# Optimization experiments

Hardware: AMD Instinct MI355X
Metric: run time of the kernel (lower is better)

Reference implementation:

```python
import jax, jax.numpy as jnp
import numpy as np

V, B, NT, EN, EMB, ODIM = 5000, 512, 50, 200, 200, 40
PERP = 30.0
BETA_TEMP = 0.2
SINKHORN_ALPHA = 20.0
WEIGHT_ECR = 250.0
ECR_ITERS = 100
SNE_ITERS = 20
EPS_DIV = 1e-16


def _pairwise_sq(x, y):
    # ||x_i||^2 + ||y_j||^2 - 2 x_i . y_j  (matches module's pairwise_euclidean_distance)
    return (jnp.sum(x * x, axis=1)[:, None] + jnp.sum(y * y, axis=1)[None, :]
            - 2.0 * (x @ y.T))


def _bn_train(x, g, b):
    # BatchNorm1d, training mode: batch statistics, biased variance
    m = x.mean(axis=0)
    v = x.var(axis=0)
    return (x - m) / jnp.sqrt(v + 1e-5) * g + b


def _snekhorn_reduce(X, proj):
    # SNEkhorn-style symmetric entropic affinity on rows of X (log-domain
    # symmetric Sinkhorn with uniform marginals), followed by a linear readout
    # to ODIM dims. X: (n, d) -> (n, ODIM).
    C = _pairwise_sq(X, X)                       # (n, n)
    n = X.shape[0]
    eps = jnp.mean(C) / jnp.log(PERP) + 1e-6     # bandwidth tied to perplexity
    log_a = -jnp.log(float(n))                   # uniform target marginal

    @jax.checkpoint
    def step(f, _):
        lse = jax.nn.logsumexp((f[None, :] - C) / eps, axis=1)
        f = 0.5 * (f + eps * (log_a - lse))      # symmetric Sinkhorn update
        return f, None

    f, _ = jax.lax.scan(step, jnp.zeros(n, C.dtype), None, length=SNE_ITERS)
    P = jnp.exp((f[:, None] + f[None, :] - C) / eps)  # (n, n) affinity
    return P @ proj                                   # (n, ODIM)


def _ecr_loss(cost):
    # ECR: entropic OT between topic and word embeddings (fixed-iteration Sinkhorn)
    Km = jnp.exp(-cost * SINKHORN_ALPHA)          # (NT, V)
    a = jnp.full((NT, 1), 1.0 / NT, cost.dtype)
    bm = jnp.full((V, 1), 1.0 / V, cost.dtype)

    def step(u, _):
        v = bm / (Km.T @ u + EPS_DIV)
        u = a / (Km @ v + EPS_DIV)
        return u, None

    u, _ = jax.lax.scan(step, jnp.full((NT, 1), 1.0 / NT, cost.dtype), None,
                        length=ECR_ITERS)
    v = bm / (Km.T @ u + EPS_DIV)
    transp = u * (Km * v.T)
    return WEIGHT_ECR * jnp.sum(transp * cost)


def setup_inputs() -> dict:
    key = jax.random.key(0)
    ks = jax.random.split(key, 12)

    def nrm(k, shape, s=0.02):
        return jax.random.normal(k, shape, jnp.float32) * s

    word_emb = jax.random.normal(ks[0], (V, EMB), jnp.float32)
    word_emb = word_emb / jnp.linalg.norm(word_emb, axis=1, keepdims=True)
    topic_emb = jax.random.normal(ks[1], (NT, EMB), jnp.float32) * 0.1
    topic_emb = topic_emb / jnp.linalg.norm(topic_emb, axis=1, keepdims=True)

    return dict(
        bow=jax.random.uniform(ks[2], (B, V), jnp.float32),
        eps_noise=jax.random.normal(ks[3], (ODIM, NT), jnp.float32),
        W1=nrm(ks[4], (EN, V)), b1=jnp.zeros(EN, jnp.float32),
        W2=nrm(ks[5], (EN, EN)), b2=jnp.zeros(EN, jnp.float32),
        Wmu=nrm(ks[6], (NT, EN)), bmu=jnp.zeros(NT, jnp.float32),
        Wlv=nrm(ks[7], (NT, EN)), blv=jnp.zeros(NT, jnp.float32),
        g_mu=jnp.ones(NT, jnp.float32), be_mu=jnp.zeros(NT, jnp.float32),
        g_lv=jnp.ones(NT, jnp.float32), be_lv=jnp.zeros(NT, jnp.float32),
        g_dec=jnp.ones(V, jnp.float32), be_dec=jnp.zeros(V, jnp.float32),
        word_emb=word_emb, topic_emb=topic_emb,
        proj_V=nrm(ks[8], (V, ODIM), 1.0),
        proj_K=nrm(ks[9], (NT, ODIM), 1.0),
    )


def reference(bow, eps_noise, W1, b1, W2, b2, Wmu, bmu, Wlv, blv,
              g_mu, be_mu, g_lv, be_lv, g_dec, be_dec,
              word_emb, topic_emb, proj_V, proj_K):
    # bow_reduced = SNEkhorn(bow.T).T : (ODIM, V)
    bow_reduced = _snekhorn_reduce(bow.T, proj_V).T

    # encoder1: Linear -> softplus -> Linear -> softplus
    e1 = jax.nn.softplus(bow_reduced @ W1.T + b1)
    e1 = jax.nn.softplus(e1 @ W2.T + b2)
    mu = _bn_train(e1 @ Wmu.T + bmu, g_mu, be_mu)        # (ODIM, NT)
    logvar = _bn_train(e1 @ Wlv.T + blv, g_lv, be_lv)

    z = mu + eps_noise * jnp.exp(0.5 * logvar)           # reparameterize (training)
    theta = jax.nn.softmax(z, axis=1)                    # (ODIM, NT)
    theta_reduced = _snekhorn_reduce(theta.T, proj_K).T  # (ODIM, NT)

    # KL vs logistic-normal prior; with a = ones: mu2 = 0, var2 = 1 - 1/NT
    var2 = 1.0 - 1.0 / NT
    var = jnp.exp(logvar)
    kld = 0.5 * ((var / var2 + mu * mu / var2 + jnp.log(var2) - logvar).sum(axis=1) - NT)
    loss_KL = kld.mean()

    # beta + decode (cost computed once; torch code computes it twice identically)
    cost = _pairwise_sq(topic_emb, word_emb)             # (NT, V)
    beta = jax.nn.softmax(-cost / BETA_TEMP, axis=0)
    recon = jax.nn.softmax(_bn_train(theta_reduced @ beta, g_dec, be_dec), axis=-1)
    recon_loss = -(bow_reduced * jnp.log(recon)).sum(axis=1).mean()

    loss_TM = recon_loss + loss_KL
    loss_ECR = _ecr_loss(cost)
    loss = loss_TM + loss_ECR
    return loss, loss_TM, loss_ECR, theta_reduced
```

## Files before the change

kernel.cpp:

```cpp
#include <hip/hip_runtime.h>
#include <hip/hip_bf16.h>
#include <hip/hip_fp16.h>

#define VV 5000
#define NTOP 50
#define ENH 200
#define NEMB 200
#define OD 40
#define MP 5120
#define KNS 5008

typedef __attribute__((ext_vector_type(8))) short short8;
typedef __attribute__((ext_vector_type(4))) float f32x4;

constexpr size_t OFF_R      = 0;
constexpr size_t OFF_S      = 20224;
constexpr size_t OFF_SCAL   = 22528;
constexpr size_t OFF_PHIA   = 22784;
constexpr size_t OFF_PHIB   = 43008;
constexpr size_t OFF_ROWS   = 63232;
constexpr size_t OFF_PARTS  = 63744;
constexpr size_t OFF_FLAGS  = 71936;
constexpr size_t OFF_MUPRE  = 72960;
constexpr size_t OFF_LVPRE  = 81152;
constexpr size_t OFF_E1T    = 89344;
constexpr size_t OFF_E2T    = 121600;
constexpr size_t OFF_THRED  = 153856;
constexpr size_t OFF_BOWRED = 162048;
constexpr size_t ZERO_BYTES = 962304;
constexpr size_t OFF_PVT    = 962304;
constexpr size_t OFF_XB     = 1453824;
constexpr size_t OFF_CE     = 6696704;
constexpr size_t OFF_COST   = 56696832;
constexpr size_t OFF_KM     = 57697024;
constexpr size_t OFF_BETA   = 58697216;
constexpr size_t OFF_RN     = 59697408;

__global__ __launch_bounds__(256) void k1_stats(const float* __restrict__ bow,
    __hip_bfloat16* __restrict__ Xb, float* __restrict__ r, float* __restrict__ s){
  __shared__ float lds[64][129];
  const int t = threadIdx.x;
  const int i0 = blockIdx.x * 128, d0 = blockIdx.y * 64;
  #pragma unroll
  for (int m = 0; m < 32; ++m){
    int idx = m*256 + t;
    int di = idx >> 7;
    int ii = idx & 127;
    int gi = i0 + ii;
    lds[di][ii] = (gi < VV) ? bow[(size_t)(d0+di)*VV + gi] : 0.f;
  }
  __syncthreads();
  if (t < 128 && (i0 + t) < VV){
    float acc = 0.f;
    for (int di = 0; di < 64; ++di){ float v = lds[di][t]; acc += v*v; }
    atomicAdd(&r[i0+t], acc);
  }
  if (t < 64){
    float acc = 0.f;
    for (int ii = 0; ii < 128; ++ii) acc += lds[t][ii];
    atomicAdd(&s[d0+t], acc);
  }
  __syncthreads();
  #pragma unroll
  for (int m = 0; m < 32; ++m){
    int idx = m*256 + t;
    int ii = idx >> 6;
    int dd = idx & 63;
    Xb[(size_t)(i0+ii)*512 + d0 + dd] = __float2bfloat16(lds[dd][ii]);
  }
}

__global__ __launch_bounds__(256) void k2_eps(const float* __restrict__ r,
    const float* __restrict__ s, float* __restrict__ scal){
  const int t = threadIdx.x;
  float a = 0.f, b = 0.f;
  for (int i = t; i < VV; i += 256) a += r[i];
  for (int d = t; d < 512; d += 256){ float v = s[d]; b += v*v; }
  #pragma unroll
  for (int off = 32; off; off >>= 1){
    a += __shfl_down(a, off, 64);
    b += __shfl_down(b, off, 64);
  }
  __shared__ float ra[4], rb[4];
  int lane = t & 63, w = t >> 6;
  if (lane == 0){ ra[w] = a; rb[w] = b; }
  __syncthreads();
  if (t == 0){
    float sa = ra[0]+ra[1]+ra[2]+ra[3];
    float sb = rb[0]+rb[1]+rb[2]+rb[3];
    float meanC = 2.f*sa/(float)VV - 2.f*sb/((float)VV*(float)VV);
    float eps = meanC / logf(30.f) + 1e-6f;
    scal[0] = eps;
    scal[1] = 1.f/eps;
  }
}

__device__ __forceinline__ void ecr_block(int b, int it_base, int n_iters, bool do_final,
    const __half* __restrict__ Kn, const float* __restrict__ cost,
    float* __restrict__ acc, int* __restrict__ cnt, float* __restrict__ scal,
    char* smem){
  __half* KmL = (__half*)smem;
  float* varr = (float*)(smem + 32208);
  float* us   = (float*)(smem + 33488);
  float* p5   = (float*)(smem + 33696);
  float* redr = (float*)(smem + 34736);
  const int t = threadIdx.x;
  const int base = (b < 8) ? b*313 : 2504 + (b-8)*312;
  const int sz   = (b < 8) ? 313 : 312;
  for (int c = t; c < 322; c += 256){
    if (c < sz){
      #pragma unroll
      for (int q = 0; q < NTOP; ++q)
        KmL[q*322 + c] = Kn[(size_t)q*KNS + base + c];
    } else {
      #pragma unroll
      for (int q = 0; q < NTOP; ++q) KmL[q*322 + c] = __float2half(0.f);
    }
  }
  if (t < 52){
    float u0 = 0.f;
    if (t < NTOP){
      if (it_base == 0) u0 = 1.f/(float)NTOP;
      else {
        float sm = __hip_atomic_load(&acc[((it_base-1)%3)*64 + t],
                                     __ATOMIC_RELAXED, __HIP_MEMORY_SCOPE_AGENT);
        u0 = (1.f/(float)NTOP)/(sm + 1e-16f);
      }
    }
    us[t] = u0;
  }
  for (int c = sz + t; c < 320; c += 256) varr[c] = 0.f;
  __syncthreads();
  const bool act = (2*t < sz);
  for (int k = 0; k < n_iters; ++k){
    const int g = it_base + k;
    if (act){
      float w0 = 0.f, w1 = 0.f, w2 = 0.f, w3 = 0.f;
      #pragma unroll
      for (int q = 0; q < NTOP; q += 2){
        float u0 = us[q], u1 = us[q+1];
        float2 f0 = __half22float2(*(const __half2*)(KmL + q*322 + 2*t));
        float2 f1 = __half22float2(*(const __half2*)(KmL + (q+1)*322 + 2*t));
        w0 += f0.x*u0; w1 += f0.y*u0;
        w2 += f1.x*u1; w3 += f1.y*u1;
      }
      float2 vv;
      vv.x = (1.f/(float)VV)/((w0+w2) + 1e-16f);
      vv.y = (2*t+1 < sz) ? (1.f/(float)VV)/((w1+w3) + 1e-16f) : 0.f;
      *(float2*)(varr + 2*t) = vv;
    }
    __syncthreads();
    if (t < 250){
      const int qq = t % NTOP, stripe = t / NTOP;
      const __half* kp = KmL + qq*322 + stripe*64;
      const float* vp = varr + stripe*64;
      float s0 = 0.f, s1 = 0.f, s2 = 0.f, s3 = 0.f;
      #pragma unroll
      for (int n = 0; n < 64; n += 4){
        float2 fa = __half22float2(*(const __half2*)(kp + n));
        float2 fb = __half22float2(*(const __half2*)(kp + n + 2));
        float4 v4 = *(const float4*)(vp + n);
        s0 += fa.x*v4.x; s1 += fa.y*v4.y; s2 += fb.x*v4.z; s3 += fb.y*v4.w;
      }
      p5[stripe*52 + qq] = (s0+s1)+(s2+s3);
    }
    __syncthreads();
    if (t < NTOP){
      float sm = p5[t] + p5[52+t] + p5[104+t] + p5[156+t] + p5[208+t];
      __hip_atomic_fetch_add(&acc[(g%3)*64 + t], sm,
                             __ATOMIC_RELAXED, __HIP_MEMORY_SCOPE_AGENT);
    }
    __asm__ volatile("s_waitcnt vmcnt(0)" ::: "memory");
    if (t == 0){
      __hip_atomic_fetch_add(cnt, 1, __ATOMIC_RELEASE, __HIP_MEMORY_SCOPE_AGENT);
      const int tgt = 16*(g+1);
      while (__hip_atomic_load(cnt, __ATOMIC_ACQUIRE, __HIP_MEMORY_SCOPE_AGENT) < tgt)
        __builtin_amdgcn_s_sleep(1);
    }
    if (t < NTOP){
      float sm = __hip_atomic_load(&acc[(g%3)*64 + t],
                                   __ATOMIC_RELAXED, __HIP_MEMORY_SCOPE_AGENT);
      us[t] = (1.f/(float)NTOP)/(sm + 1e-16f);
    }
    if (t < 64)
      __hip_atomic_store(&acc[((g+2)%3)*64 + t], 0.f,
                         __ATOMIC_RELAXED, __HIP_MEMORY_SCOPE_AGENT);
    __syncthreads();
  }
  if (!do_final) return;
  float lsum = 0.f;
  if (act){
    float w0 = 0.f, w1 = 0.f, w2 = 0.f, w3 = 0.f;
    #pragma unroll
    for (int q = 0; q < NTOP; q += 2){
      float u0 = us[q], u1 = us[q+1];
      float2 f0 = __half22float2(*(const __half2*)(KmL + q*322 + 2*t));
      float2 f1 = __half22float2(*(const __half2*)(KmL + (q+1)*322 + 2*t));
      w0 += f0.x*u0; w1 += f0.y*u0;
      w2 += f1.x*u1; w3 += f1.y*u1;
    }
    float v0 = (1.f/(float)VV)/((w0+w2) + 1e-16f);
    const bool ok1 = (2*t+1 < sz);
    float v1 = ok1 ? (1.f/(float)VV)/((w1+w3) + 1e-16f) : 0.f;
    float accv = 0.f;
    #pragma unroll
    for (int q = 0; q < NTOP; ++q){
      float2 f = __half22float2(*(const __half2*)(KmL + q*322 + 2*t));
      float uq = us[q];
      float c0 = cost[(size_t)q*VV + base + 2*t];
      accv += uq*f.x*v0*c0;
      if (ok1){
        float c1 = cost[(size_t)q*VV + base + 2*t + 1];
        accv += uq*f.y*v1*c1;
      }
    }
    lsum = accv;
  }
  #pragma unroll
  for (int off = 32; off; off >>= 1) lsum += __shfl_down(lsum, off, 64);
  if ((t & 63) == 0) redr[t >> 6] = lsum;
  __syncthreads();
  if (t == 0) atomicAdd(&scal[3], redr[0]+redr[1]+redr[2]+redr[3]);
}

__global__ __launch_bounds__(256) void k3_gemm_ecr(const __hip_bfloat16* __restrict__ Xb,
    const float* __restrict__ r, float* __restrict__ scal, __half* __restrict__ Ce,
    const __half* __restrict__ Kn, const float* __restrict__ cost,
    float* __restrict__ accg, int* __restrict__ cnt){
  __shared__ __align__(16) char smem[36864];
  if (blockIdx.x < 16){
    ecr_block(blockIdx.x, 0, 12, false, Kn, cost, accg, cnt, scal, smem);
    return;
  }
  __hip_bfloat16* As = (__hip_bfloat16*)smem;
  __hip_bfloat16* Bs = (__hip_bfloat16*)(smem + 128*72*2);
  const int b2 = blockIdx.x - 16;
  const int t = threadIdx.x;
  const int i0 = (b2 % 40) * 128, j0 = (b2 / 40) * 128;
  const int lane = t & 63, w = t >> 6;
  const int wr = w >> 1, wc = w & 1;
  const int m16 = lane & 15, q4 = lane >> 4;
  f32x4 acc[4][4];
  #pragma unroll
  for (int a = 0; a < 4; ++a)
    #pragma unroll
    for (int b = 0; b < 4; ++b) acc[a][b] = (f32x4){0.f,0.f,0.f,0.f};
  const int srow = t >> 3, sseg = t & 7;
  for (int kc = 0; kc < 512; kc += 64){
    __syncthreads();
    #pragma unroll
    for (int m = 0; m < 4; ++m){
      int row = m*32 + srow;
      uint4 va = *(const uint4*)(Xb + (size_t)(i0+row)*512 + kc + sseg*8);
      *(uint4*)(As + row*72 + sseg*8) = va;
      uint4 vb = *(const uint4*)(Xb + (size_t)(j0+row)*512 + kc + sseg*8);
      *(uint4*)(Bs + row*72 + sseg*8) = vb;
    }
    __syncthreads();
    #pragma unroll
    for (int ks = 0; ks < 64; ks += 32){
      short8 af[4], bf[4];
      #pragma unroll
      for (int f = 0; f < 4; ++f){
        af[f] = *(const short8*)(As + (wr*64 + f*16 + m16)*72 + ks + q4*8);
        bf[f] = *(const short8*)(Bs + (wc*64 + f*16 + m16)*72 + ks + q4*8);
      }
      #pragma unroll
      for (int fr = 0; fr < 4; ++fr)
        #pragma unroll
        for (int fc = 0; fc < 4; ++fc)
          acc[fr][fc] = __builtin_amdgcn_mfma_f32_16x16x32_bf16(af[fr], bf[fc], acc[fr][fc], 0, 0, 0);
    }
  }
  const float inv_eps = scal[1];
  #pragma unroll
  for (int fr = 0; fr < 4; ++fr){
    int rbase = i0 + wr*64 + fr*16 + q4*4;
    #pragma unroll
    for (int fc = 0; fc < 4; ++fc){
      int col = j0 + wc*64 + fc*16 + m16;
      if (col < VV){
        float rc = r[col];
        #pragma unroll
        for (int q = 0; q < 4; ++q){
          int row = rbase + q;
          if (row < VV){
            float val = (r[row] + rc - 2.f*acc[fr][fc][q]) * inv_eps;
            Ce[(size_t)row*VV + col] = __float2half(val);
          }
        }
      }
    }
  }
}

__global__ __launch_bounds__(256) void k4_sweep_ecr(const __half* __restrict__ Ce,
    const float* __restrict__ phi_in, float* __restrict__ phi_out,
    const __half* __restrict__ Kn, const float* __restrict__ cost,
    float* __restrict__ accg, int* __restrict__ cnt, float* __restrict__ scal,
    int it_base, int n_ecr){
  __shared__ __align__(16) char smem[34752];
  const int t = threadIdx.x;
  if (blockIdx.x < 16){
    ecr_block(blockIdx.x, it_base, n_ecr, it_base + n_ecr == 100,
              Kn, cost, accg, cnt, scal, smem);
    return;
  }
  const int i0 = (blockIdx.x - 16) * 4;
  float acc[4] = {0.f, 0.f, 0.f, 0.f};
  const uint4* ce0 = (const uint4*)(Ce + (size_t)i0*VV);
  for (int u = t; u < 625; u += 256){
    float4 p0 = *(const float4*)(phi_in + u*8);
    float4 p1 = *(const float4*)(phi_in + u*8 + 4);
    #pragma unroll
    for (int rr = 0; rr < 4; ++rr){
      uint4 v = ce0[(size_t)rr*625 + u];
      const __half2* hp = (const __half2*)&v;
      float2 c0 = __half22float2(hp[0]);
      float2 c1 = __half22float2(hp[1]);
      float2 c2 = __half22float2(hp[2]);
      float2 c3 = __half22float2(hp[3]);
      acc[rr] += __expf(p0.x - c0.x) + __expf(p0.y - c0.y)
               + __expf(p0.z - c1.x) + __expf(p0.w - c1.y)
               + __expf(p1.x - c2.x) + __expf(p1.y - c2.y)
               + __expf(p1.z - c3.x) + __expf(p1.w - c3.y);
    }
  }
  #pragma unroll
  for (int rr = 0; rr < 4; ++rr)
    #pragma unroll
    for (int off = 32; off; off >>= 1)
      acc[rr] += __shfl_down(acc[rr], off, 64);
  float* red = (float*)smem;
  int lane = t & 63, w = t >> 6;
  if (lane == 0){
    #pragma unroll
    for (int rr = 0; rr < 4; ++rr) red[w*4 + rr] = acc[rr];
  }
  __syncthreads();
  if (t < 4){
    float ssum = red[t] + red[4+t] + red[8+t] + red[12+t];
    const float loga = -8.517193191416238f;
    phi_out[i0 + t] = 0.5f*(phi_in[i0 + t] + loga - __logf(ssum));
  }
}

__global__ __launch_bounds__(256) void k5p_pvt(const float* __restrict__ projV,
    __hip_bfloat16* __restrict__ pvt){
  int idx = blockIdx.x*256 + threadIdx.x;
  if (idx >= 48*MP) return;
  int n = idx / MP, j = idx - n*MP;
  float v = (n < OD && j < VV) ? projV[(size_t)j*OD + n] : 0.f;
  pvt[idx] = __float2bfloat16(v);
}

__global__ __launch_bounds__(256) void k5_bowred(const __half* __restrict__ Ce,
    const float* __restrict__ phi, const __hip_bfloat16* __restrict__ pvt,
    float* __restrict__ brpA, float* __restrict__ brpB){
  __shared__ __align__(16) char smem[25600];
  __hip_bfloat16* As = (__hip_bfloat16*)smem;
  __hip_bfloat16* Bs = (__hip_bfloat16*)(smem + 18432);
  const int t = threadIdx.x;
  const int i0 = blockIdx.x * 128;
  const int k0 = blockIdx.y * 640;
  const int lane = t & 63, w = t >> 6;
  const int m16 = lane & 15, q4 = lane >> 4;
  f32x4 acc[2][3];
  #pragma unroll
  for (int a = 0; a < 2; ++a)
    #pragma unroll
    for (int b = 0; b < 3; ++b) acc[a][b] = (f32x4){0.f,0.f,0.f,0.f};
  for (int kc = k0; kc < k0 + 640; kc += 64){
    __syncthreads();
    #pragma unroll
    for (int m = 0; m < 4; ++m){
      int g = m*256 + t;
      int row = g >> 3, cg = g & 7;
      int gi = i0 + row, j2 = kc + cg*8;
      union { __hip_bfloat16 h[8]; short8 v; } u;
      if (gi < VV && j2 < VV){
        uint4 vce = *(const uint4*)(Ce + (size_t)gi*VV + j2);
        const __half2* hp = (const __half2*)&vce;
        float pb = phi[gi];
        float4 pj0 = *(const float4*)(phi + j2);
        float4 pj1 = *(const float4*)(phi + j2 + 4);
        float pj[8] = {pj0.x,pj0.y,pj0.z,pj0.w,pj1.x,pj1.y,pj1.z,pj1.w};
        #pragma unroll
        for (int e = 0; e < 4; ++e){
          float2 ce = __half22float2(hp[e]);
          u.h[2*e]   = __float2bfloat16(__expf(pb + pj[2*e]   - ce.x));
          u.h[2*e+1] = __float2bfloat16(__expf(pb + pj[2*e+1] - ce.y));
        }
      } else {
        #pragma unroll
        for (int e = 0; e < 8; ++e) u.h[e] = __float2bfloat16(0.f);
      }
      *(short8*)(As + row*72 + cg*8) = u.v;
    }
    #pragma unroll
    for (int m = 0; m < 12; ++m){
      int idx = m*256 + t;
      int row = idx >> 6, c = idx & 63;
      Bs[row*72 + c] = pvt[(size_t)row*MP + kc + c];
    }
    __syncthreads();
    #pragma unroll
    for (int ks = 0; ks < 64; ks += 32){
      short8 af[2], bf[3];
      #pragma unroll
      for (int f = 0; f < 2; ++f)
        af[f] = *(const short8*)(As + (w*32 + f*16 + m16)*72 + ks + q4*8);
      #pragma unroll
      for (int f = 0; f < 3; ++f)
        bf[f] = *(const short8*)(Bs + (f*16 + m16)*72 + ks + q4*8);
      #pragma unroll
      for (int fr = 0; fr < 2; ++fr)
        #pragma unroll
        for (int fc = 0; fc < 3; ++fc)
          acc[fr][fc] = __builtin_amdgcn_mfma_f32_16x16x32_bf16(af[fr], bf[fc], acc[fr][fc], 0, 0, 0);
    }
  }
  __syncthreads();
  float* LF = (float*)smem;
  #pragma unroll
  for (int fr = 0; fr < 2; ++fr){
    int lr = w*32 + fr*16 + q4*4;
    #pragma unroll
    for (int fc = 0; fc < 3; ++fc){
      int col = fc*16 + m16;
      #pragma unroll
      for (int q = 0; q < 4; ++q)
        LF[col*133 + lr + q] = acc[fr][fc][q];
    }
  }
  __syncthreads();
  float* brp = (blockIdx.y < 6) ? brpA + (size_t)blockIdx.y*200000
                                : brpB + (size_t)(blockIdx.y - 6)*200000;
  for (int o = t; o < OD*128; o += 256){
    int col = o >> 7, row = o & 127;
    int gr = i0 + row;
    if (gr < VV) brp[(size_t)col*VV + gr] = LF[col*133 + row];
  }
}

__global__ __launch_bounds__(256) void k5r_red(const float* __restrict__ brpA,
    const float* __restrict__ brpB, float* __restrict__ br){
  int idx = blockIdx.x*256 + threadIdx.x;
  if (idx >= 50000) return;
  const float4* a = (const float4*)brpA;
  const float4* b = (const float4*)brpB;
  float4 s = a[idx];
  #pragma unroll
  for (int sl = 1; sl < 6; ++sl){
    float4 v = a[(size_t)sl*50000 + idx];
    s.x += v.x; s.y += v.y; s.z += v.z; s.w += v.w;
  }
  #pragma unroll
  for (int sl = 0; sl < 2; ++sl){
    float4 v = b[(size_t)sl*50000 + idx];
    s.x += v.x; s.y += v.y; s.z += v.z; s.w += v.w;
  }
  ((float4*)br)[idx] = s;
}

__global__ __launch_bounds__(256) void k6_e1(const float* __restrict__ br,
    const float* __restrict__ W1, float* __restrict__ e1pre){
  const int t = threadIdx.x;
  const int lane = t & 63, w = t >> 6;
  const int k = blockIdx.x*4 + w;
  const int f0 = blockIdx.y * 125;
  float acc[OD];
  #pragma unroll
  for (int i = 0; i < OD; ++i) acc[i] = 0.f;
  const float4* w4p = (const float4*)(W1 + (size_t)k*VV);
  for (int f4 = f0 + lane; f4 < f0 + 125; f4 += 64){
    float4 wv = w4p[f4];
    #pragma unroll
    for (int i = 0; i < OD; ++i){
      float4 bv = ((const float4*)(br + (size_t)i*VV))[f4];
      acc[i] += bv.x*wv.x + bv.y*wv.y + bv.z*wv.z + bv.w*wv.w;
    }
  }
  #pragma unroll
  for (int i = 0; i < OD; ++i)
    #pragma unroll
    for (int off = 32; off; off >>= 1)
      acc[i] += __shfl_down(acc[i], off, 64);
  __shared__ float red[4][OD];
  if (lane == 0){
    #pragma unroll
    for (int i = 0; i < OD; ++i) red[w][i] = acc[i];
  }
  __syncthreads();
  if (t < 160){
    int ww = t / OD, i = t - ww*OD;
    int kk = blockIdx.x*4 + ww;
    atomicAdd(&e1pre[kk*OD + i], red[ww][i]);
  }
}

__global__ __launch_bounds__(256) void k6b_sp(const float* __restrict__ b1,
    float* __restrict__ e1t){
  int idx = blockIdx.x*256 + threadIdx.x;
  if (idx >= ENH*OD) return;
  int kk = idx / OD;
  float x = e1t[idx] + b1[kk];
  e1t[idx] = (x > 20.f) ? x : log1pf(__expf(x));
}

__global__ __launch_bounds__(256) void k7_e2(const float* __restrict__ e1t,
    const float* __restrict__ W2, const float* __restrict__ b2, float* __restrict__ e2t){
  const int t = threadIdx.x;
  const int lane = t & 63, w = t >> 6;
  const int k = blockIdx.x*4 + w;
  float acc[OD];
  #pragma unroll
  for (int i = 0; i < OD; ++i) acc[i] = 0.f;
  for (int j = lane; j < ENH; j += 64){
    float wv = W2[(size_t)k*ENH + j];
    #pragma unroll
    for (int i = 0; i < OD; ++i) acc[i] += e1t[j*OD + i] * wv;
  }
  #pragma unroll
  for (int i = 0; i < OD; ++i)
    #pragma unroll
    for (int off = 32; off; off >>= 1)
      acc[i] += __shfl_down(acc[i], off, 64);
  __shared__ float red[4][OD];
  if (lane == 0){
    #pragma unroll
    for (int i = 0; i < OD; ++i) red[w][i] = acc[i];
  }
  __syncthreads();
  if (t < 160){
    int ww = t / OD, i = t - ww*OD;
    int kk = blockIdx.x*4 + ww;
    float x = red[ww][i] + b2[kk];
    float sp = (x > 20.f) ? x : log1pf(__expf(x));
    e2t[kk*OD + i] = sp;
  }
}

__global__ __launch_bounds__(256) void k8a_mulv(const float* __restrict__ e2t,
    const float* __restrict__ Wmu, const float* __restrict__ bmu,
    const float* __restrict__ Wlv, const float* __restrict__ blv,
    float* __restrict__ mupre, float* __restrict__ lvpre){
  int id = blockIdx.x*256 + threadIdx.x;
  if (id >= NTOP*OD) return;
  int t50 = id / OD, i = id - t50*OD;
  float am = 0.f, al = 0.f;
  for (int kk = 0; kk < ENH; ++kk){
    float e = e2t[kk*OD + i];
    am += e * Wmu[t50*ENH + kk];
    al += e * Wlv[t50*ENH + kk];
  }
  mupre[t50*OD + i] = am + bmu[t50];
  lvpre[t50*OD + i] = al + blv[t50];
}

__global__ __launch_bounds__(256) void k8b_theta(const float* __restrict__ mupre,
    const float* __restrict__ lvpre,
    const float* __restrict__ g_mu, const float* __restrict__ be_mu,
    const float* __restrict__ g_lv, const float* __restrict__ be_lv,
    const float* __restrict__ eps_noise, const float* __restrict__ projK,
    float* __restrict__ thred, float* __restrict__ d_out3, float* __restrict__ scal){
  __shared__ float mu[NTOP][OD];
  __shared__ float lv[NTOP][OD];
  __shared__ float th[OD][NTOP];
  __shared__ float C2[NTOP][NTOP];
  __shared__ float P2[NTOP][NTOP];
  __shared__ float f2[NTOP], nf[NTOP];
  __shared__ float sred[4];
  __shared__ float eps2s[2];
  const int t = threadIdx.x;
  if (t < NTOP){
    float m = 0.f;
    for (int i = 0; i < OD; ++i) m += mupre[t*OD + i];
    m *= (1.f/OD);
    float v = 0.f;
    for (int i = 0; i < OD; ++i){ float d = mupre[t*OD+i] - m; v += d*d; }
    v *= (1.f/OD);
    float sc = g_mu[t] * rsqrtf(v + 1e-5f);
    float sh = be_mu[t];
    for (int i = 0; i < OD; ++i) mu[t][i] = (mupre[t*OD+i] - m)*sc + sh;
    m = 0.f;
    for (int i = 0; i < OD; ++i) m += lvpre[t*OD + i];
    m *= (1.f/OD);
    v = 0.f;
    for (int i = 0; i < OD; ++i){ float d = lvpre[t*OD+i] - m; v += d*d; }
    v *= (1.f/OD);
    sc = g_lv[t] * rsqrtf(v + 1e-5f);
    sh = be_lv[t];
    for (int i = 0; i < OD; ++i) lv[t][i] = (lvpre[t*OD+i] - m)*sc + sh;
  }
  __syncthreads();
  {
    float kl = 0.f;
    if (t < OD){
      const float var2 = 1.f - 1.f/(float)NTOP;
      const float lv2 = logf(var2);
      float ssum = 0.f;
      for (int q = 0; q < NTOP; ++q){
        float l = lv[q][t];
        float m = mu[q][t];
        ssum += (__expf(l) + m*m)/var2 + lv2 - l;
      }
      kl = 0.5f*(ssum - (float)NTOP);
    }
    #pragma unroll
    for (int off = 32; off; off >>= 1) kl += __shfl_down(kl, off, 64);
    if ((t & 63) == 0) sred[t >> 6] = kl;
    __syncthreads();
    if (t == 0) scal[2] = (sred[0]+sred[1]+sred[2]+sred[3]) * (1.f/OD);
    __syncthreads();
  }
  if (t < OD){
    float z[NTOP];
    float mx = -1e30f;
    for (int q = 0; q < NTOP; ++q){
      float val = mu[q][t] + eps_noise[t*NTOP + q]*__expf(0.5f*lv[q][t]);
      z[q] = val;
      mx = fmaxf(mx, val);
    }
    float ssum = 0.f;
    for (int q = 0; q < NTOP; ++q){ float e = __expf(z[q]-mx); z[q] = e; ssum += e; }
    float inv = 1.f/ssum;
    for (int q = 0; q < NTOP; ++q) th[t][q] = z[q]*inv;
  }
  __syncthreads();
  {
    float csum = 0.f;
    for (int pr = t; pr < NTOP*NTOP; pr += 256){
      int a = pr / NTOP, b = pr - (pr/NTOP)*NTOP;
      float ss = 0.f;
      for (int i = 0; i < OD; ++i){ float d = th[i][a] - th[i][b]; ss += d*d; }
      C2[a][b] = ss;
      csum += ss;
    }
    #pragma unroll
    for (int off = 32; off; off >>= 1) csum += __shfl_down(csum, off, 64);
    if ((t & 63) == 0) sred[t >> 6] = csum;
    __syncthreads();
    if (t == 0){
      float meanC = (sred[0]+sred[1]+sred[2]+sred[3]) / ((float)NTOP*NTOP);
      float e2 = meanC / logf(30.f) + 1e-6f;
      eps2s[0] = e2; eps2s[1] = 1.f/e2;
    }
  }
  if (t < NTOP) f2[t] = 0.f;
  __syncthreads();
  const float loga2 = -logf((float)NTOP);
  for (int it = 0; it < 20; ++it){
    if (t < NTOP){
      float ie = eps2s[1];
      float ssum = 0.f;
      for (int sI = 0; sI < NTOP; ++sI)
        ssum += __expf((f2[sI] - C2[t][sI]) * ie);
      float lse = __logf(ssum);
      nf[t] = 0.5f*(f2[t] + eps2s[0]*(loga2 - lse));
    }
    __syncthreads();
    if (t < NTOP) f2[t] = nf[t];
    __syncthreads();
  }
  for (int pr = t; pr < NTOP*NTOP; pr += 256){
    int a = pr / NTOP, b = pr - (pr/NTOP)*NTOP;
    P2[a][b] = __expf((f2[a] + f2[b] - C2[a][b]) * eps2s[1]);
  }
  __syncthreads();
  for (int o = t; o < NTOP*OD; o += 256){
    int t50 = o / OD, kk = o - (o/OD)*OD;
    float ssum = 0.f;
    for (int sI = 0; sI < NTOP; ++sI)
      ssum += P2[t50][sI] * projK[sI*OD + kk];
    thred[kk*NTOP + t50] = ssum;
    d_out3[kk*NTOP + t50] = ssum;
  }
}

__global__ __launch_bounds__(256) void k10_cost(const float* __restrict__ temb,
    const float* __restrict__ wemb, float* __restrict__ cost, __half* __restrict__ Kn,
    float* __restrict__ beta){
  __shared__ float Tt[100][52];
  __shared__ float wed[100][68];
  __shared__ float sc[52][64];
  __shared__ float tn[52];
  __shared__ float wn[64];
  const int t = threadIdx.x;
  const int j0 = blockIdx.x * 64;
  const int tg = t >> 4, jg = t & 15;
  float am[4][4];
  #pragma unroll
  for (int a = 0; a < 4; ++a)
    #pragma unroll
    for (int b = 0; b < 4; ++b) am[a][b] = 0.f;
  float tnp = 0.f, wnp = 0.f;
  for (int c = 0; c < 2; ++c){
    __syncthreads();
    const int dbase = c*100;
    for (int idx = t; idx < NTOP*100; idx += 256){
      int t50 = idx / 100, d = idx - t50*100;
      Tt[d][t50] = temb[t50*NEMB + dbase + d];
    }
    for (int idx = t; idx < 64*100; idx += 256){
      int j = idx / 100, d = idx - j*100;
      int gj = j0 + j;
      wed[d][j] = (gj < VV) ? wemb[(size_t)gj*NEMB + dbase + d] : 0.f;
    }
    __syncthreads();
    if (t < NTOP){
      float a = 0.f;
      for (int d = 0; d < 100; ++d){ float v = Tt[d][t]; a += v*v; }
      tnp += a;
    }
    if (t >= 64 && t < 128){
      int j = t - 64;
      float a = 0.f;
      for (int d = 0; d < 100; ++d){ float v = wed[d][j]; a += v*v; }
      wnp += a;
    }
    if (t < 208){
      for (int d = 0; d < 100; ++d){
        const float4 tv = *(const float4*)(&Tt[d][tg*4]);
        const float4 wv = *(const float4*)(&wed[d][jg*4]);
        am[0][0] += tv.x*wv.x; am[0][1] += tv.x*wv.y; am[0][2] += tv.x*wv.z; am[0][3] += tv.x*wv.w;
        am[1][0] += tv.y*wv.x; am[1][1] += tv.y*wv.y; am[1][2] += tv.y*wv.z; am[1][3] += tv.y*wv.w;
        am[2][0] += tv.z*wv.x; am[2][1] += tv.z*wv.y; am[2][2] += tv.z*wv.z; am[2][3] += tv.z*wv.w;
        am[3][0] += tv.w*wv.x; am[3][1] += tv.w*wv.y; am[3][2] += tv.w*wv.z; am[3][3] += tv.w*wv.w;
      }
    }
  }
  if (t < NTOP) tn[t] = tnp;
  if (t >= 64 && t < 128) wn[t-64] = wnp;
  __syncthreads();
  if (t < 208){
    #pragma unroll
    for (int a = 0; a < 4; ++a){
      int t50 = tg*4 + a;
      if (t50 < NTOP){
        float tv = tn[t50];
        float cc[4];
        #pragma unroll
        for (int b = 0; b < 4; ++b) cc[b] = tv + wn[jg*4+b] - 2.f*am[a][b];
        int gj = j0 + jg*4;
        if (gj + 3 < VV)
          *(float4*)(cost + (size_t)t50*VV + gj) = make_float4(cc[0],cc[1],cc[2],cc[3]);
        #pragma unroll
        for (int b = 0; b < 4; ++b) sc[t50][jg*4+b] = -5.f*cc[b];
      }
    }
  }
  __syncthreads();
  if (t < 64){
    int gj = j0 + t;
    if (gj < VV){
      float mx = -1e30f;
      for (int q = 0; q < NTOP; ++q) mx = fmaxf(mx, sc[q][t]);
      float ssum = 0.f;
      for (int q = 0; q < NTOP; ++q){ float e = __expf(sc[q][t]-mx); sc[q][t] = e; ssum += e; }
      float inv = 1.f/ssum;
      for (int q = 0; q < NTOP; ++q){
        float e = sc[q][t];
        float e2 = e*e;
        Kn[(size_t)q*KNS + gj] = __float2half(e2*e2);
        beta[(size_t)q*VV + gj] = e*inv;
      }
    }
  }
}

__global__ __launch_bounds__(256) void k12_reconA(const float* __restrict__ thred,
    const float* __restrict__ beta, const float* __restrict__ g_dec,
    const float* __restrict__ be_dec, float* __restrict__ Rn){
  __shared__ float trs[OD][NTOP];
  const int t = threadIdx.x;
  for (int o = t; o < OD*NTOP; o += 256) trs[o/NTOP][o - (o/NTOP)*NTOP] = thred[o];
  __syncthreads();
  int j = blockIdx.x*256 + t;
  if (j >= VV) return;
  float a[OD];
  #pragma unroll
  for (int i = 0; i < OD; ++i) a[i] = 0.f;
  for (int q = 0; q < NTOP; ++q){
    float bv = beta[(size_t)q*VV + j];
    #pragma unroll
    for (int i = 0; i < OD; ++i) a[i] += trs[i][q]*bv;
  }
  float m = 0.f;
  #pragma unroll
  for (int i = 0; i < OD; ++i) m += a[i];
  m *= (1.f/OD);
  float v = 0.f;
  #pragma unroll
  for (int i = 0; i < OD; ++i){ float d = a[i]-m; v += d*d; }
  v *= (1.f/OD);
  float scale = g_dec[j]*rsqrtf(v + 1e-5f);
  float sh = be_dec[j];
  #pragma unroll
  for (int i = 0; i < OD; ++i) Rn[(size_t)i*VV + j] = (a[i]-m)*scale + sh;
}

__global__ __launch_bounds__(256) void k13_reconB(const float* __restrict__ Rn,
    const float* __restrict__ br, float* __restrict__ rows){
  const int i = blockIdx.x;
  const int t = threadIdx.x;
  float s1 = 0.f, s2 = 0.f, s3 = 0.f;
  for (int j = t; j < VV; j += 256){
    float rn = Rn[(size_t)i*VV + j];
    float bv = br[(size_t)i*VV + j];
    s1 += __expf(rn);
    s2 += bv*rn;
    s3 += bv;
  }
  #pragma unroll
  for (int off = 32; off; off >>= 1){
    s1 += __shfl_down(s1, off, 64);
    s2 += __shfl_down(s2, off, 64);
    s3 += __shfl_down(s3, off, 64);
  }
  __shared__ float red[3][4];
  int lane = t & 63, w = t >> 6;
  if (lane == 0){ red[0][w] = s1; red[1][w] = s2; red[2][w] = s3; }
  __syncthreads();
  if (t == 0){
    rows[i]      = red[0][0]+red[0][1]+red[0][2]+red[0][3];
    rows[40 + i] = red[1][0]+red[1][1]+red[1][2]+red[1][3];
    rows[80 + i] = red[2][0]+red[2][1]+red[2][2]+red[2][3];
  }
}

__global__ void k14_final(const float* __restrict__ rows, const float* __restrict__ scal,
    float* __restrict__ out){
  const int t = threadIdx.x;
  float v = 0.f;
  if (t < OD) v = rows[40 + t] - logf(rows[t]) * rows[80 + t];
  #pragma unroll
  for (int off = 32; off; off >>= 1) v += __shfl_down(v, off, 64);
  if (t == 0){
    float recon = -v * (1.f/OD);
    float tm = recon + scal[2];
    float ecr = 250.f * scal[3];
    out[0] = tm + ecr;
    out[1] = tm;
    out[2] = ecr;
  }
}

extern "C" void kernel_launch(void* const* d_in, const int* in_sizes, int n_in,
                              void* d_out, int out_size, void* d_ws, size_t ws_size,
                              hipStream_t stream){
  const float* bow   = (const float*)d_in[0];
  const float* epsn  = (const float*)d_in[1];
  const float* W1    = (const float*)d_in[2];
  const float* b1    = (const float*)d_in[3];
  const float* W2    = (const float*)d_in[4];
  const float* b2    = (const float*)d_in[5];
  const float* Wmu   = (const float*)d_in[6];
  const float* bmu   = (const float*)d_in[7];
  const float* Wlv   = (const float*)d_in[8];
  const float* blv   = (const float*)d_in[9];
  const float* g_mu  = (const float*)d_in[10];
  const float* be_mu = (const float*)d_in[11];
  const float* g_lv  = (const float*)d_in[12];
  const float* be_lv = (const float*)d_in[13];
  const float* g_dec = (const float*)d_in[14];
  const float* be_dec= (const float*)d_in[15];
  const float* wemb  = (const float*)d_in[16];
  const float* temb  = (const float*)d_in[17];
  const float* projV = (const float*)d_in[18];
  const float* projK = (const float*)d_in[19];
  char* ws = (char*)d_ws;
  float* r     = (float*)(ws + OFF_R);
  float* s     = (float*)(ws + OFF_S);
  float* scal  = (float*)(ws + OFF_SCAL);
  float* phiA  = (float*)(ws + OFF_PHIA);
  float* phiB  = (float*)(ws + OFF_PHIB);
  float* rows  = (float*)(ws + OFF_ROWS);
  float* accg  = (float*)(ws + OFF_PARTS);
  int*   cnt   = (int*)(ws + OFF_FLAGS);
  float* mupre = (float*)(ws + OFF_MUPRE);
  float* lvpre = (float*)(ws + OFF_LVPRE);
  float* e1t   = (float*)(ws + OFF_E1T);
  float* e2t   = (float*)(ws + OFF_E2T);
  float* thred = (float*)(ws + OFF_THRED);
  float* br    = (float*)(ws + OFF_BOWRED);
  __hip_bfloat16* pvt = (__hip_bfloat16*)(ws + OFF_PVT);
  __hip_bfloat16* Xb  = (__hip_bfloat16*)(ws + OFF_XB);
  __half* Ce   = (__half*)(ws + OFF_CE);
  float* cost  = (float*)(ws + OFF_COST);
  __half* Kn   = (__half*)(ws + OFF_KM);
  float* beta  = (float*)(ws + OFF_BETA);
  float* Rn    = (float*)(ws + OFF_RN);
  float* brpA  = (float*)(ws + OFF_XB);
  float* brpB  = (float*)(ws + OFF_COST);
  float* out   = (float*)d_out;

  hipMemsetAsync(d_ws, 0, ZERO_BYTES, stream);
  k10_cost<<<79, 256, 0, stream>>>(temb, wemb, cost, Kn, beta);
  k1_stats<<<dim3(40, 8), 256, 0, stream>>>(bow, Xb, r, s);
  k2_eps<<<1, 256, 0, stream>>>(r, s, scal);
  k3_gemm_ecr<<<1616, 256, 0, stream>>>(Xb, r, scal, Ce, Kn, cost, accg, cnt);
  {
    float* pin = phiA; float* pout = phiB;
    int itb = 12;
    for (int itr = 0; itr < 20; ++itr){
      int n = (itr < 12) ? 4 : 5;
      k4_sweep_ecr<<<1266, 256, 0, stream>>>(Ce, pin, pout, Kn, cost, accg, cnt,
                                             scal, itb, n);
      itb += n;
      float* tmp = pin; pin = pout; pout = tmp;
    }
  }
  k5p_pvt<<<960, 256, 0, stream>>>(projV, pvt);
  k5_bowred<<<dim3(40, 8), 256, 0, stream>>>(Ce, phiA, pvt, brpA, brpB);
  k5r_red<<<196, 256, 0, stream>>>(brpA, brpB, br);
  k6_e1<<<dim3(50, 10), 256, 0, stream>>>(br, W1, e1t);
  k6b_sp<<<32, 256, 0, stream>>>(b1, e1t);
  k7_e2<<<50, 256, 0, stream>>>(e1t, W2, b2, e2t);
  k8a_mulv<<<8, 256, 0, stream>>>(e2t, Wmu, bmu, Wlv, blv, mupre, lvpre);
  k8b_theta<<<1, 256, 0, stream>>>(mupre, lvpre, g_mu, be_mu, g_lv, be_lv,
                                   epsn, projK, thred, out + 3, scal);
  k12_reconA<<<20, 256, 0, stream>>>(thred, beta, g_dec, be_dec, Rn);
  k13_reconB<<<40, 256, 0, stream>>>(Rn, br, rows);
  k14_final<<<1, 64, 0, stream>>>(rows, scal, out);
}
```

Baseline: 845.8 us.

## Redistribute ECR Sinkhorn iterations across more kernels and widen sweep rows per block

```diff
diff --git a/kernel.cpp b/kernel.cpp
--- a/kernel.cpp
+++ b/kernel.cpp
@@ -36,65 +36,6 @@
 constexpr size_t OFF_BETA   = 58697216;
 constexpr size_t OFF_RN     = 59697408;
 
-__global__ __launch_bounds__(256) void k1_stats(const float* __restrict__ bow,
-    __hip_bfloat16* __restrict__ Xb, float* __restrict__ r, float* __restrict__ s){
-  __shared__ float lds[64][129];
-  const int t = threadIdx.x;
-  const int i0 = blockIdx.x * 128, d0 = blockIdx.y * 64;
-  #pragma unroll
-  for (int m = 0; m < 32; ++m){
-    int idx = m*256 + t;
-    int di = idx >> 7;
-    int ii = idx & 127;
-    int gi = i0 + ii;
-    lds[di][ii] = (gi < VV) ? bow[(size_t)(d0+di)*VV + gi] : 0.f;
-  }
-  __syncthreads();
-  if (t < 128 && (i0 + t) < VV){
-    float acc = 0.f;
-    for (int di = 0; di < 64; ++di){ float v = lds[di][t]; acc += v*v; }
-    atomicAdd(&r[i0+t], acc);
-  }
-  if (t < 64){
-    float acc = 0.f;
-    for (int ii = 0; ii < 128; ++ii) acc += lds[t][ii];
-    atomicAdd(&s[d0+t], acc);
-  }
-  __syncthreads();
-  #pragma unroll
-  for (int m = 0; m < 32; ++m){
-    int idx = m*256 + t;
-    int ii = idx >> 6;
-    int dd = idx & 63;
-    Xb[(size_t)(i0+ii)*512 + d0 + dd] = __float2bfloat16(lds[dd][ii]);
-  }
-}
-
-__global__ __launch_bounds__(256) void k2_eps(const float* __restrict__ r,
-    const float* __restrict__ s, float* __restrict__ scal){
-  const int t = threadIdx.x;
-  float a = 0.f, b = 0.f;
-  for (int i = t; i < VV; i += 256) a += r[i];
-  for (int d = t; d < 512; d += 256){ float v = s[d]; b += v*v; }
-  #pragma unroll
-  for (int off = 32; off; off >>= 1){
-    a += __shfl_down(a, off, 64);
-    b += __shfl_down(b, off, 64);
-  }
-  __shared__ float ra[4], rb[4];
-  int lane = t & 63, w = t >> 6;
-  if (lane == 0){ ra[w] = a; rb[w] = b; }
-  __syncthreads();
-  if (t == 0){
-    float sa = ra[0]+ra[1]+ra[2]+ra[3];
-    float sb = rb[0]+rb[1]+rb[2]+rb[3];
-    float meanC = 2.f*sa/(float)VV - 2.f*sb/((float)VV*(float)VV);
-    float eps = meanC / logf(30.f) + 1e-6f;
-    scal[0] = eps;
-    scal[1] = 1.f/eps;
-  }
-}
-
 __device__ __forceinline__ void ecr_block(int b, int it_base, int n_iters, bool do_final,
     const __half* __restrict__ Kn, const float* __restrict__ cost,
     float* __restrict__ acc, int* __restrict__ cnt, float* __restrict__ scal,
@@ -223,13 +164,80 @@
   if (t == 0) atomicAdd(&scal[3], redr[0]+redr[1]+redr[2]+redr[3]);
 }
 
+__global__ __launch_bounds__(256) void k1_stats(const float* __restrict__ bow,
+    __hip_bfloat16* __restrict__ Xb, float* __restrict__ r, float* __restrict__ s,
+    const __half* __restrict__ Kn, const float* __restrict__ cost,
+    float* __restrict__ accg, int* __restrict__ cnt, float* __restrict__ scal){
+  __shared__ __align__(16) char smem[34816];
+  const int t = threadIdx.x;
+  if (blockIdx.x >= 40){
+    int b = (blockIdx.x - 40)*8 + blockIdx.y;
+    ecr_block(b, 0, 15, false, Kn, cost, accg, cnt, scal, smem);
+    return;
+  }
+  float (*lds)[129] = (float(*)[129])smem;
+  const int i0 = blockIdx.x * 128, d0 = blockIdx.y * 64;
+  #pragma unroll
+  for (int m = 0; m < 32; ++m){
+    int idx = m*256 + t;
+    int di = idx >> 7;
+    int ii = idx & 127;
+    int gi = i0 + ii;
+    lds[di][ii] = (gi < VV) ? bow[(size_t)(d0+di)*VV + gi] : 0.f;
+  }
+  __syncthreads();
+  if (t < 128 && (i0 + t) < VV){
+    float acc = 0.f;
+    for (int di = 0; di < 64; ++di){ float v = lds[di][t]; acc += v*v; }
+    atomicAdd(&r[i0+t], acc);
+  }
+  if (t < 64){
+    float acc = 0.f;
+    for (int ii = 0; ii < 128; ++ii) acc += lds[t][ii];
+    atomicAdd(&s[d0+t], acc);
+  }
+  __syncthreads();
+  #pragma unroll
+  for (int m = 0; m < 32; ++m){
+    int idx = m*256 + t;
+    int ii = idx >> 6;
+    int dd = idx & 63;
+    Xb[(size_t)(i0+ii)*512 + d0 + dd] = __float2bfloat16(lds[dd][ii]);
+  }
+}
+
+__global__ __launch_bounds__(256) void k2_eps(const float* __restrict__ r,
+    const float* __restrict__ s, float* __restrict__ scal){
+  const int t = threadIdx.x;
+  float a = 0.f, b = 0.f;
+  for (int i = t; i < VV; i += 256) a += r[i];
+  for (int d = t; d < 512; d += 256){ float v = s[d]; b += v*v; }
+  #pragma unroll
+  for (int off = 32; off; off >>= 1){
+    a += __shfl_down(a, off, 64);
+    b += __shfl_down(b, off, 64);
+  }
+  __shared__ float ra[4], rb[4];
+  int lane = t & 63, w = t >> 6;
+  if (lane == 0){ ra[w] = a; rb[w] = b; }
+  __syncthreads();
+  if (t == 0){
+    float sa = ra[0]+ra[1]+ra[2]+ra[3];
+    float sb = rb[0]+rb[1]+rb[2]+rb[3];
+    float meanC = 2.f*sa/(float)VV - 2.f*sb/((float)VV*(float)VV);
+    float eps = meanC / logf(30.f) + 1e-6f;
+    scal[0] = eps;
+    scal[1] = 1.f/eps;
+  }
+}
+
 __global__ __launch_bounds__(256) void k3_gemm_ecr(const __hip_bfloat16* __restrict__ Xb,
     const float* __restrict__ r, float* __restrict__ scal, __half* __restrict__ Ce,
     const __half* __restrict__ Kn, const float* __restrict__ cost,
     float* __restrict__ accg, int* __restrict__ cnt){
   __shared__ __align__(16) char smem[36864];
   if (blockIdx.x < 16){
-    ecr_block(blockIdx.x, 0, 12, false, Kn, cost, accg, cnt, scal, smem);
+    ecr_block(blockIdx.x, 15, 25, false, Kn, cost, accg, cnt, scal, smem);
     return;
   }
   __hip_bfloat16* As = (__hip_bfloat16*)smem;
@@ -298,22 +306,23 @@
     const float* __restrict__ phi_in, float* __restrict__ phi_out,
     const __half* __restrict__ Kn, const float* __restrict__ cost,
     float* __restrict__ accg, int* __restrict__ cnt, float* __restrict__ scal,
-    int it_base, int n_ecr){
-  __shared__ __align__(16) char smem[34752];
+    int it_base){
+  __shared__ __align__(16) char smem[34816];
   const int t = threadIdx.x;
   if (blockIdx.x < 16){
-    ecr_block(blockIdx.x, it_base, n_ecr, it_base + n_ecr == 100,
-              Kn, cost, accg, cnt, scal, smem);
+    ecr_block(blockIdx.x, it_base, 2, false, Kn, cost, accg, cnt, scal, smem);
     return;
   }
-  const int i0 = (blockIdx.x - 16) * 4;
-  float acc[4] = {0.f, 0.f, 0.f, 0.f};
+  const int i0 = (blockIdx.x - 16) * 8;
+  float acc[8];
+  #pragma unroll
+  for (int rr = 0; rr < 8; ++rr) acc[rr] = 0.f;
   const uint4* ce0 = (const uint4*)(Ce + (size_t)i0*VV);
   for (int u = t; u < 625; u += 256){
     float4 p0 = *(const float4*)(phi_in + u*8);
     float4 p1 = *(const float4*)(phi_in + u*8 + 4);
     #pragma unroll
-    for (int rr = 0; rr < 4; ++rr){
+    for (int rr = 0; rr < 8; ++rr){
       uint4 v = ce0[(size_t)rr*625 + u];
       const __half2* hp = (const __half2*)&v;
       float2 c0 = __half22float2(hp[0]);
@@ -327,7 +336,7 @@
     }
   }
   #pragma unroll
-  for (int rr = 0; rr < 4; ++rr)
+  for (int rr = 0; rr < 8; ++rr)
     #pragma unroll
     for (int off = 32; off; off >>= 1)
       acc[rr] += __shfl_down(acc[rr], off, 64);
@@ -335,11 +344,11 @@
   int lane = t & 63, w = t >> 6;
   if (lane == 0){
     #pragma unroll
-    for (int rr = 0; rr < 4; ++rr) red[w*4 + rr] = acc[rr];
-  }
-  __syncthreads();
-  if (t < 4){
-    float ssum = red[t] + red[4+t] + red[8+t] + red[12+t];
+    for (int rr = 0; rr < 8; ++rr) red[w*8 + rr] = acc[rr];
+  }
+  __syncthreads();
+  if (t < 8){
+    float ssum = red[t] + red[8+t] + red[16+t] + red[24+t];
     const float loga = -8.517193191416238f;
     phi_out[i0 + t] = 0.5f*(phi_in[i0 + t] + loga - __logf(ssum));
   }
@@ -356,11 +365,18 @@
 
 __global__ __launch_bounds__(256) void k5_bowred(const __half* __restrict__ Ce,
     const float* __restrict__ phi, const __hip_bfloat16* __restrict__ pvt,
-    float* __restrict__ brpA, float* __restrict__ brpB){
-  __shared__ __align__(16) char smem[25600];
+    float* __restrict__ brpA, float* __restrict__ brpC, float* __restrict__ brpD,
+    const __half* __restrict__ Kn, const float* __restrict__ cost,
+    float* __restrict__ accg, int* __restrict__ cnt, float* __restrict__ scal){
+  __shared__ __align__(16) char smem[34816];
+  const int t = threadIdx.x;
+  if (blockIdx.x >= 40){
+    int b = (blockIdx.x - 40)*8 + blockIdx.y;
+    ecr_block(b, 80, 15, false, Kn, cost, accg, cnt, scal, smem);
+    return;
+  }
   __hip_bfloat16* As = (__hip_bfloat16*)smem;
   __hip_bfloat16* Bs = (__hip_bfloat16*)(smem + 18432);
-  const int t = threadIdx.x;
   const int i0 = blockIdx.x * 128;
   const int k0 = blockIdx.y * 640;
   const int lane = t & 63, w = t >> 6;
@@ -435,7 +451,7 @@
   }
   __syncthreads();
   float* brp = (blockIdx.y < 6) ? brpA + (size_t)blockIdx.y*200000
-                                : brpB + (size_t)(blockIdx.y - 6)*200000;
+             : (blockIdx.y == 6) ? brpC : brpD;
   for (int o = t; o < OD*128; o += 256){
     int col = o >> 7, row = o & 127;
     int gr = i0 + row;
@@ -444,28 +460,39 @@
 }
 
 __global__ __launch_bounds__(256) void k5r_red(const float* __restrict__ brpA,
-    const float* __restrict__ brpB, float* __restrict__ br){
+    const float* __restrict__ brpC, const float* __restrict__ brpD,
+    float* __restrict__ br){
   int idx = blockIdx.x*256 + threadIdx.x;
   if (idx >= 50000) return;
   const float4* a = (const float4*)brpA;
-  const float4* b = (const float4*)brpB;
   float4 s = a[idx];
   #pragma unroll
   for (int sl = 1; sl < 6; ++sl){
     float4 v = a[(size_t)sl*50000 + idx];
     s.x += v.x; s.y += v.y; s.z += v.z; s.w += v.w;
   }
-  #pragma unroll
-  for (int sl = 0; sl < 2; ++sl){
-    float4 v = b[(size_t)sl*50000 + idx];
+  {
+    float4 v = ((const float4*)brpC)[idx];
     s.x += v.x; s.y += v.y; s.z += v.z; s.w += v.w;
   }
+  {
+    float4 v = ((const float4*)brpD)[idx];
+    s.x += v.x; s.y += v.y; s.z += v.z; s.w += v.w;
+  }
   ((float4*)br)[idx] = s;
 }
 
 __global__ __launch_bounds__(256) void k6_e1(const float* __restrict__ br,
-    const float* __restrict__ W1, float* __restrict__ e1pre){
-  const int t = threadIdx.x;
+    const float* __restrict__ W1, float* __restrict__ e1pre,
+    const __half* __restrict__ Kn, const float* __restrict__ cost,
+    float* __restrict__ accg, int* __restrict__ cnt, float* __restrict__ scal){
+  __shared__ __align__(16) char smem[34816];
+  const int t = threadIdx.x;
+  if (blockIdx.y == 10){
+    if (blockIdx.x < 16)
+      ecr_block(blockIdx.x, 95, 5, true, Kn, cost, accg, cnt, scal, smem);
+    return;
+  }
   const int lane = t & 63, w = t >> 6;
   const int k = blockIdx.x*4 + w;
   const int f0 = blockIdx.y * 125;
@@ -486,7 +513,7 @@
     #pragma unroll
     for (int off = 32; off; off >>= 1)
       acc[i] += __shfl_down(acc[i], off, 64);
-  __shared__ float red[4][OD];
+  float (*red)[OD] = (float(*)[OD])smem;
   if (lane == 0){
     #pragma unroll
     for (int i = 0; i < OD; ++i) red[w][i] = acc[i];
@@ -892,29 +919,28 @@
   float* beta  = (float*)(ws + OFF_BETA);
   float* Rn    = (float*)(ws + OFF_RN);
   float* brpA  = (float*)(ws + OFF_XB);
-  float* brpB  = (float*)(ws + OFF_COST);
+  float* brpC  = (float*)(ws + OFF_RN);
+  float* brpD  = (float*)(ws + OFF_BOWRED);
   float* out   = (float*)d_out;
 
   hipMemsetAsync(d_ws, 0, ZERO_BYTES, stream);
   k10_cost<<<79, 256, 0, stream>>>(temb, wemb, cost, Kn, beta);
-  k1_stats<<<dim3(40, 8), 256, 0, stream>>>(bow, Xb, r, s);
+  k1_stats<<<dim3(42, 8), 256, 0, stream>>>(bow, Xb, r, s, Kn, cost, accg, cnt, scal);
   k2_eps<<<1, 256, 0, stream>>>(r, s, scal);
   k3_gemm_ecr<<<1616, 256, 0, stream>>>(Xb, r, scal, Ce, Kn, cost, accg, cnt);
   {
     float* pin = phiA; float* pout = phiB;
-    int itb = 12;
     for (int itr = 0; itr < 20; ++itr){
-      int n = (itr < 12) ? 4 : 5;
-      k4_sweep_ecr<<<1266, 256, 0, stream>>>(Ce, pin, pout, Kn, cost, accg, cnt,
-                                             scal, itb, n);
-      itb += n;
+      k4_sweep_ecr<<<641, 256, 0, stream>>>(Ce, pin, pout, Kn, cost, accg, cnt,
+                                            scal, 40 + 2*itr);
       float* tmp = pin; pin = pout; pout = tmp;
     }
   }
   k5p_pvt<<<960, 256, 0, stream>>>(projV, pvt);
-  k5_bowred<<<dim3(40, 8), 256, 0, stream>>>(Ce, phiA, pvt, brpA, brpB);
-  k5r_red<<<196, 256, 0, stream>>>(brpA, brpB, br);
-  k6_e1<<<dim3(50, 10), 256, 0, stream>>>(br, W1, e1t);
+  k5_bowred<<<dim3(42, 8), 256, 0, stream>>>(Ce, phiA, pvt, brpA, brpC, brpD,
+                                             Kn, cost, accg, cnt, scal);
+  k5r_red<<<196, 256, 0, stream>>>(brpA, brpC, brpD, br);
+  k6_e1<<<dim3(50, 11), 256, 0, stream>>>(br, W1, e1t, Kn, cost, accg, cnt, scal);
   k6b_sp<<<32, 256, 0, stream>>>(b1, e1t);
   k7_e2<<<50, 256, 0, stream>>>(e1t, W2, b2, e2t);
   k8a_mulv<<<8, 256, 0, stream>>>(e2t, Wmu, bmu, Wlv, blv, mupre, lvpre);
```

Result: faster. 800.4 us (-5.4%).
